# Kernel optimization log

Hardware: AMD Instinct MI355X
Metric: run time of the kernel (lower is better)

Reference implementation:

```python
import jax, jax.numpy as jnp
import numpy as np

D_MODEL = 1024
HIDDEN = 4096
NUM_EXPERTS = 8
NUM_GROUPS = 4      # from _compute_group_size(4, 4096) with max_group_size=4096
GROUP_SIZE = 4096
EXPERT_CAPACITY = 512  # round(1.0 * 4096 / 8), >= max(8, 4096//100)


def setup_inputs() -> dict:
    key = jax.random.key(0)
    ks = jax.random.split(key, 10)
    s_in = 1.0 / np.sqrt(D_MODEL)
    s_hid = 1.0 / np.sqrt(HIDDEN)
    return {
        "x": jax.random.normal(ks[0], (4, 4096, D_MODEL), dtype=jnp.float32),
        "gate_w": jax.random.normal(ks[1], (D_MODEL, NUM_EXPERTS), dtype=jnp.float32) * 0.1,
        "gate_b": jax.random.normal(ks[2], (NUM_EXPERTS,), dtype=jnp.float32) * 0.01,
        "temperature": jnp.ones((1,), dtype=jnp.float32),
        "shared_w1": jax.random.normal(ks[3], (D_MODEL, HIDDEN), dtype=jnp.float32) * s_in,
        "shared_b1": jnp.zeros((HIDDEN,), dtype=jnp.float32),
        "shared_w2": jax.random.normal(ks[4], (HIDDEN, D_MODEL), dtype=jnp.float32) * s_hid,
        "shared_b2": jnp.zeros((D_MODEL,), dtype=jnp.float32),
        "expert_w1": jax.random.normal(ks[5], (NUM_EXPERTS, D_MODEL, HIDDEN), dtype=jnp.float32) * s_in,
        "expert_b1": jnp.zeros((NUM_EXPERTS, HIDDEN), dtype=jnp.float32),
        "expert_w2": jax.random.normal(ks[6], (NUM_EXPERTS, HIDDEN, D_MODEL), dtype=jnp.float32) * s_hid,
        "expert_b2": jnp.zeros((NUM_EXPERTS, D_MODEL), dtype=jnp.float32),
    }


def reference(x, gate_w, gate_b, temperature, shared_w1, shared_b1, shared_w2,
              shared_b2, expert_w1, expert_b1, expert_w2, expert_b2):
    B, S, D = x.shape
    T = NUM_GROUPS * GROUP_SIZE  # total tokens (no padding here)
    xg = x.reshape(NUM_GROUPS, GROUP_SIZE, D)

    # Router: softmax over temperature-scaled gate logits
    logits = jnp.einsum('gsd,de->gse', xg, gate_w) + gate_b
    safe_temp = jnp.maximum(temperature, 0.1)
    probs = jax.nn.softmax(logits / safe_temp, axis=-1)  # [G, Gs, E]
    # per-expert top-k over ALL tokens (flattened across groups)
    flat_probs = probs.transpose(2, 0, 1).reshape(NUM_EXPERTS, T)
    scores, tok_idx = jax.lax.top_k(flat_probs, EXPERT_CAPACITY)  # [E, C]

    # Shared expert FFN (gelu is tanh-approx, matching flax nn.gelu default)
    shared = jnp.einsum('gsh,hd->gsd',
                        jax.nn.gelu(jnp.einsum('gsd,dh->gsh', xg, shared_w1) + shared_b1),
                        shared_w2) + shared_b2

    # Routed experts: gather tokens, grouped FFN, weighted scatter-add
    x_flat = xg.reshape(T, D)
    tokens = x_flat[tok_idx]  # [E, C, D]
    h = jax.nn.gelu(jnp.einsum('ecd,edh->ech', tokens, expert_w1) + expert_b1[:, None, :])
    out_e = jnp.einsum('ech,ehd->ecd', h, expert_w2) + expert_b2[:, None, :]
    out_e = out_e * scores[..., None]
    routed = jnp.zeros_like(x_flat).at[tok_idx.reshape(-1)].add(out_e.reshape(-1, D))

    out = shared.reshape(T, D) + routed
    return out.reshape(B, S, D)
```

## Files before the change

kernel.cpp:

```cpp
#include <hip/hip_runtime.h>

#define NTOK 16384
#define DMODEL 1024
#define DHID 4096
#define NEXP 8
#define CAP 512

typedef __attribute__((ext_vector_type(8))) short bfrag_t;
typedef __attribute__((ext_vector_type(4))) float ffrag_t;
typedef __attribute__((ext_vector_type(4))) unsigned int u32x4;

__device__ __forceinline__ unsigned short f2bf(float f) {
  unsigned u = __float_as_uint(f);
  u += 0x7FFFu + ((u >> 16) & 1u);
  return (unsigned short)(u >> 16);
}

__device__ __forceinline__ float gelu_fast(float x) {
  float t = x * x;
  float z = x * fmaf(0.071354814f, t, 1.5957691f);
  float e = __expf(-z);
  return x * __builtin_amdgcn_rcpf(1.0f + e);
}

__global__ __launch_bounds__(256) void k_trans_all(const float* __restrict__ sw1,
                                                   const float* __restrict__ ew1,
                                                   const float* __restrict__ sw2,
                                                   const float* __restrict__ ew2,
                                                   unsigned short* __restrict__ w1t,
                                                   unsigned short* __restrict__ ew1t,
                                                   unsigned short* __restrict__ w2t,
                                                   unsigned short* __restrict__ ew2t) {
  const int zb = blockIdx.z;
  const float* in;
  unsigned short* out;
  int K, N, bx, by;
  if (zb < 9) {
    K = DMODEL; N = DHID;
    bx = blockIdx.x; by = blockIdx.y;
    if (zb == 0) { in = sw1; out = w1t; }
    else { in = ew1 + (size_t)(zb - 1) * K * N; out = ew1t + (size_t)(zb - 1) * N * K; }
  } else {
    K = DHID; N = DMODEL;
    const int id = blockIdx.y * 64 + blockIdx.x;
    bx = id & 15; by = id >> 4;
    if (zb == 9) { in = sw2; out = w2t; }
    else { in = ew2 + (size_t)(zb - 10) * K * N; out = ew2t + (size_t)(zb - 10) * N * K; }
  }
  __shared__ float tile[64][65];
  const int n0 = bx * 64, k0 = by * 64;
  const int tx = threadIdx.x & 63, ty = threadIdx.x >> 6;
#pragma unroll
  for (int i = 0; i < 16; ++i) {
    const int k = ty * 16 + i;
    tile[k][tx] = in[(size_t)(k0 + k) * N + n0 + tx];
  }
  __syncthreads();
  const int sx = threadIdx.x & 7, sy = threadIdx.x >> 3;
#pragma unroll
  for (int j = 0; j < 2; ++j) {
    const int n = sy + j * 32;
    u32x4 v;
    v.x = (unsigned)f2bf(tile[sx * 8 + 0][n]) | ((unsigned)f2bf(tile[sx * 8 + 1][n]) << 16);
    v.y = (unsigned)f2bf(tile[sx * 8 + 2][n]) | ((unsigned)f2bf(tile[sx * 8 + 3][n]) << 16);
    v.z = (unsigned)f2bf(tile[sx * 8 + 4][n]) | ((unsigned)f2bf(tile[sx * 8 + 5][n]) << 16);
    v.w = (unsigned)f2bf(tile[sx * 8 + 6][n]) | ((unsigned)f2bf(tile[sx * 8 + 7][n]) << 16);
    *(u32x4*)&out[(size_t)(n0 + n) * K + k0 + sx * 8] = v;
  }
}

__global__ __launch_bounds__(256) void k_router(const float* __restrict__ x, const float* __restrict__ gw,
                                                const float* __restrict__ gb, const float* __restrict__ temp,
                                                float* __restrict__ probs, unsigned short* __restrict__ xb) {
  __shared__ float gws[DMODEL * NEXP];
  for (int i = threadIdx.x; i < DMODEL * NEXP; i += 256) gws[i] = gw[i];
  __syncthreads();
  const int wave = threadIdx.x >> 6, lane = threadIdx.x & 63;
  const int t = blockIdx.x * 4 + wave;
  const float* xr = x + (size_t)t * DMODEL;
  unsigned short* xw = xb + (size_t)t * DMODEL;
  float acc[NEXP];
#pragma unroll
  for (int e = 0; e < NEXP; ++e) acc[e] = 0.f;
  for (int d = lane; d < DMODEL; d += 64) {
    float xv = xr[d];
    xw[d] = f2bf(xv);
#pragma unroll
    for (int e = 0; e < NEXP; ++e) acc[e] += xv * gws[d * NEXP + e];
  }
#pragma unroll
  for (int off = 32; off >= 1; off >>= 1) {
#pragma unroll
    for (int e = 0; e < NEXP; ++e) acc[e] += __shfl_xor(acc[e], off);
  }
  if (lane == 0) {
    float st = fmaxf(temp[0], 0.1f);
    float m = -1e30f;
#pragma unroll
    for (int e = 0; e < NEXP; ++e) { acc[e] = (acc[e] + gb[e]) / st; m = fmaxf(m, acc[e]); }
    float s = 0.f;
#pragma unroll
    for (int e = 0; e < NEXP; ++e) { acc[e] = expf(acc[e] - m); s += acc[e]; }
    float inv = 1.f / s;
#pragma unroll
    for (int e = 0; e < NEXP; ++e) probs[(size_t)e * NTOK + t] = acc[e] * inv;
  }
}

__global__ __launch_bounds__(1024) void k_topk(const float* __restrict__ probs, int* __restrict__ tok,
                                               float* __restrict__ scores, int* __restrict__ eqbuf,
                                               int* __restrict__ slot) {
  const int e = blockIdx.x;
  const float* p = probs + (size_t)e * NTOK;
  int* eq = eqbuf + (size_t)e * NTOK;
  int* sl = slot + (size_t)e * NTOK;
  __shared__ int hist[256];
  __shared__ unsigned sh_pref;
  __shared__ int sh_k, sh_gt, sh_eq, sh_cnt;
  const int tid = threadIdx.x;
  const int NTHR = 1024;
  for (int t = tid; t < NTOK; t += NTHR) sl[t] = -1;
  if (tid == 0) { sh_pref = 0u; sh_k = CAP; }
  __syncthreads();
  for (int pass = 3; pass >= 0; --pass) {
    if (tid < 256) hist[tid] = 0;
    __syncthreads();
    const unsigned pref = sh_pref;
    const int shift = pass * 8;
    for (int t = tid; t < NTOK; t += NTHR) {
      unsigned key = __float_as_uint(p[t]);
      bool cand = (pass == 3) || ((key >> (shift + 8)) == pref);
      if (cand) atomicAdd(&hist[(key >> shift) & 255], 1);
    }
    __syncthreads();
    if (tid == 0) {
      int k = sh_k;
      int d = 255;
      while (hist[d] < k) { k -= hist[d]; --d; }
      sh_k = k;
      sh_pref = (pref << 8) | (unsigned)d;
    }
    __syncthreads();
  }
  const unsigned Kstar = sh_pref;
  const int need_eq = sh_k;
  if (tid == 0) { sh_gt = 0; sh_eq = 0; }
  __syncthreads();
  for (int t = tid; t < NTOK; t += NTHR) {
    unsigned key = __float_as_uint(p[t]);
    if (key > Kstar) {
      int pos = atomicAdd(&sh_gt, 1);
      tok[e * CAP + pos] = t;
      scores[e * CAP + pos] = p[t];
      sl[t] = pos;
    } else if (key == Kstar) {
      int q = atomicAdd(&sh_eq, 1);
      eq[q] = t;
    }
  }
  __syncthreads();
  const int cg = sh_gt, ce = sh_eq;
  if (ce <= need_eq) {
    for (int j = tid; j < ce; j += NTHR) {
      tok[e * CAP + cg + j] = eq[j];
      scores[e * CAP + cg + j] = p[eq[j]];
      sl[eq[j]] = cg + j;
    }
  } else {
    int lo = 0, hi = NTOK - 1;
    while (lo < hi) {
      int mid = (lo + hi) >> 1;
      if (tid == 0) sh_cnt = 0;
      __syncthreads();
      for (int j = tid; j < ce; j += NTHR)
        if (eq[j] <= mid) atomicAdd(&sh_cnt, 1);
      __syncthreads();
      if (sh_cnt >= need_eq) hi = mid; else lo = mid + 1;
      __syncthreads();
    }
    if (tid == 0) sh_cnt = 0;
    __syncthreads();
    for (int j = tid; j < ce; j += NTHR) {
      if (eq[j] <= lo) {
        int pos = cg + atomicAdd(&sh_cnt, 1);
        tok[e * CAP + pos] = eq[j];
        scores[e * CAP + pos] = p[eq[j]];
        sl[eq[j]] = pos;
      }
    }
  }
}

template <int MODE, bool GATHER, bool NT>
__global__ __launch_bounds__(256, 4) void k_gemm(
    const unsigned short* __restrict__ A, const unsigned short* __restrict__ Bt,
    const float* __restrict__ bias, float* __restrict__ outF, unsigned short* __restrict__ outB,
    const int* __restrict__ tok, const float* __restrict__ scale,
    int M, int N, int Kloop, int LDK, int ksplit) {
  const int zb = blockIdx.z / ksplit;
  const int kc = blockIdx.z % ksplit;
  if (!GATHER) A += (size_t)zb * M * LDK;
  A += (size_t)kc * Kloop;
  Bt += (size_t)zb * N * LDK + (size_t)kc * Kloop;
  const float* bz = bias + (size_t)zb * N;

  const int gx = gridDim.x, gy = gridDim.y;
  const int nwg = gx * gy;
  const int id = blockIdx.x + blockIdx.y * gx;
  int bx, by;
  if ((gx & 7) == 0) {
    const int x = id & 7, c = id >> 3, H = gx >> 3;
    bx = x * H + (c % H);
    by = c / H;
  } else if ((nwg & 7) == 0) {
    const int q = nwg >> 3;
    const int sw = (id & 7) * q + (id >> 3);
    bx = sw % gx;
    by = sw / gx;
  } else {
    bx = blockIdx.x;
    by = blockIdx.y;
  }
  const int m0 = bx * 128, n0 = by * 128;

  const int tid = threadIdx.x, wave = tid >> 6, lane = tid & 63;
  const int wm = (wave >> 1) * 64, wn = (wave & 1) * 64;

  __shared__ alignas(16) unsigned short sh[128 * 128];
  unsigned short* As = sh;
  unsigned short* Bs = sh + 128 * 64;

  ffrag_t acc[4][4];
#pragma unroll
  for (int i = 0; i < 4; ++i)
#pragma unroll
    for (int j = 0; j < 4; ++j)
#pragma unroll
      for (int r = 0; r < 4; ++r) acc[i][j][r] = 0.f;

  int lb[4];
  const unsigned short* rowA[4];
  const unsigned short* rowB[4];
#pragma unroll
  for (int it = 0; it < 4; ++it) {
    int L = it * 256 + tid;
    int rr = L >> 3;
    int gg = (L & 7) ^ (rr & 7);
    lb[it] = (it * 256 + wave * 64) * 16;
    const unsigned short* ab =
        GATHER ? (A + (size_t)tok[zb * M + m0 + rr] * LDK) : (A + (size_t)(m0 + rr) * LDK);
    rowA[it] = ab + gg * 8;
    rowB[it] = Bt + (size_t)(n0 + rr) * LDK + gg * 8;
  }

  for (int kt = 0; kt < Kloop; kt += 64) {
#pragma unroll
    for (int it = 0; it < 4; ++it) {
      __builtin_amdgcn_global_load_lds(
          (const __attribute__((address_space(1))) unsigned int*)(rowA[it] + kt),
          (__attribute__((address_space(3))) unsigned int*)((char*)As + lb[it]), 16, 0, 0);
      __builtin_amdgcn_global_load_lds(
          (const __attribute__((address_space(1))) unsigned int*)(rowB[it] + kt),
          (__attribute__((address_space(3))) unsigned int*)((char*)Bs + lb[it]), 16, 0, 0);
    }
    __syncthreads();
#pragma unroll
    for (int kk = 0; kk < 2; ++kk) {
      bfrag_t af[4], bf[4];
      const int gl = kk * 4 + (lane >> 4);
#pragma unroll
      for (int mi = 0; mi < 4; ++mi) {
        int r = wm + mi * 16 + (lane & 15);
        af[mi] = *(const bfrag_t*)&As[r * 64 + ((gl ^ (r & 7)) * 8)];
      }
#pragma unroll
      for (int ni = 0; ni < 4; ++ni) {
        int r = wn + ni * 16 + (lane & 15);
        bf[ni] = *(const bfrag_t*)&Bs[r * 64 + ((gl ^ (r & 7)) * 8)];
      }
#pragma unroll
      for (int mi = 0; mi < 4; ++mi)
#pragma unroll
        for (int ni = 0; ni < 4; ++ni)
          acc[mi][ni] = __builtin_amdgcn_mfma_f32_16x16x32_bf16(af[mi], bf[ni], acc[mi][ni], 0, 0, 0);
    }
    __syncthreads();
  }

  const int rsub = (lane >> 4) * 4, cs = lane & 15;
  if (MODE == 0) {
    float bv[4];
#pragma unroll
    for (int ni = 0; ni < 4; ++ni) bv[ni] = bz[n0 + wn + ni * 16 + cs];
#pragma unroll
    for (int mi = 0; mi < 4; ++mi)
#pragma unroll
      for (int ni = 0; ni < 4; ++ni)
#pragma unroll
        for (int r = 0; r < 4; ++r) {
          float v = acc[mi][ni][r] + bv[ni];
          sh[(wm + mi * 16 + rsub + r) * 128 + (wn + ni * 16 + cs)] = f2bf(gelu_fast(v));
        }
    __syncthreads();
    const int seg = tid & 15, rw = tid >> 4;
#pragma unroll
    for (int rep = 0; rep < 8; ++rep) {
      const int row = rep * 16 + rw;
      u32x4 v = *(const u32x4*)&sh[row * 128 + seg * 8];
      u32x4* dst = (u32x4*)&outB[((size_t)zb * M + m0 + row) * N + n0 + seg * 8];
      if (NT)
        __builtin_nontemporal_store(v, dst);
      else
        *dst = v;
    }
  } else if (MODE == 3) {
    float* po = outF + (size_t)blockIdx.z * M * N;
#pragma unroll
    for (int ni = 0; ni < 4; ++ni) {
      const int n = n0 + wn + ni * 16 + cs;
      const float bv = (kc == 0) ? bz[n] : 0.f;
#pragma unroll
      for (int mi = 0; mi < 4; ++mi)
#pragma unroll
        for (int r = 0; r < 4; ++r) {
          const int m = m0 + wm + mi * 16 + rsub + r;
          const float s = scale[zb * M + m];
          po[(size_t)m * N + n] = (acc[mi][ni][r] + bv) * s;
        }
    }
  } else {
    const int* slot = tok;
    const float* pe = scale;
    float bv[4];
#pragma unroll
    for (int ni = 0; ni < 4; ++ni) bv[ni] = bz[n0 + wn + ni * 16 + cs];
#pragma unroll
    for (int mi = 0; mi < 4; ++mi) {
#pragma unroll
      for (int r = 0; r < 4; ++r) {
        const int m = m0 + wm + mi * 16 + rsub + r;
        float ex[4] = {0.f, 0.f, 0.f, 0.f};
#pragma unroll
        for (int e = 0; e < NEXP; ++e) {
          const int sl = slot[(size_t)e * NTOK + m];
          if (sl >= 0) {
            const float* p0 = pe + ((size_t)(e * 2 + 0) * CAP + sl) * DMODEL;
            const float* p1 = pe + ((size_t)(e * 2 + 1) * CAP + sl) * DMODEL;
#pragma unroll
            for (int ni = 0; ni < 4; ++ni) {
              const int n = n0 + wn + ni * 16 + cs;
              ex[ni] += p0[n] + p1[n];
            }
          }
        }
#pragma unroll
        for (int ni = 0; ni < 4; ++ni) {
          const int n = n0 + wn + ni * 16 + cs;
          __builtin_nontemporal_store(acc[mi][ni][r] + bv[ni] + ex[ni],
                                      &outF[(size_t)m * N + n]);
        }
      }
    }
  }
}

extern "C" void kernel_launch(void* const* d_in, const int* in_sizes, int n_in,
                              void* d_out, int out_size, void* d_ws, size_t ws_size,
                              hipStream_t stream) {
  const float* x      = (const float*)d_in[0];
  const float* gate_w = (const float*)d_in[1];
  const float* gate_b = (const float*)d_in[2];
  const float* temp   = (const float*)d_in[3];
  const float* sw1    = (const float*)d_in[4];
  const float* sb1    = (const float*)d_in[5];
  const float* sw2    = (const float*)d_in[6];
  const float* sb2    = (const float*)d_in[7];
  const float* ew1    = (const float*)d_in[8];
  const float* eb1    = (const float*)d_in[9];
  const float* ew2    = (const float*)d_in[10];
  const float* eb2    = (const float*)d_in[11];
  float* out = (float*)d_out;

  char* ws = (char*)d_ws;
  size_t o = 0;
  auto take = [&](size_t bytes) { char* p = ws + o; o += (bytes + 255) & ~(size_t)255; return p; };
  unsigned short* x_bf = (unsigned short*)take((size_t)NTOK * DMODEL * 2);
  unsigned short* w1t  = (unsigned short*)take((size_t)DMODEL * DHID * 2);
  unsigned short* w2t  = (unsigned short*)take((size_t)DHID * DMODEL * 2);
  unsigned short* ew1t = (unsigned short*)take((size_t)NEXP * DMODEL * DHID * 2);
  unsigned short* ew2t = (unsigned short*)take((size_t)NEXP * DHID * DMODEL * 2);
  float* probs         = (float*)take((size_t)NEXP * NTOK * 4);
  int* tok             = (int*)take((size_t)NEXP * CAP * 4);
  float* scores        = (float*)take((size_t)NEXP * CAP * 4);
  int* eqbuf           = (int*)take((size_t)NEXP * NTOK * 4);
  int* slot            = (int*)take((size_t)NEXP * NTOK * 4);
  float* pe            = (float*)take((size_t)NEXP * 2 * CAP * DMODEL * 4);
  unsigned short* he   = (unsigned short*)take((size_t)NEXP * CAP * DHID * 2);
  unsigned short* hs   = (unsigned short*)take((size_t)NTOK * DHID * 2);

  k_trans_all<<<dim3(64, 16, 18), 256, 0, stream>>>(sw1, ew1, sw2, ew2, w1t, ew1t, w2t, ew2t);

  k_router<<<NTOK / 4, 256, 0, stream>>>(x, gate_w, gate_b, temp, probs, x_bf);
  k_topk<<<NEXP, 1024, 0, stream>>>(probs, tok, scores, eqbuf, slot);

  k_gemm<0, false, false><<<dim3(128, 32, 1), 256, 0, stream>>>(
      x_bf, w1t, sb1, nullptr, hs, nullptr, nullptr, NTOK, DHID, DMODEL, DMODEL, 1);

  k_gemm<0, true, false><<<dim3(4, 32, NEXP), 256, 0, stream>>>(
      x_bf, ew1t, eb1, nullptr, he, tok, nullptr, CAP, DHID, DMODEL, DMODEL, 1);
  k_gemm<3, false, false><<<dim3(4, 8, NEXP * 2), 256, 0, stream>>>(
      he, ew2t, eb2, pe, nullptr, nullptr, scores, CAP, DMODEL, DHID / 2, DHID, 2);

  k_gemm<4, false, true><<<dim3(128, 8, 1), 256, 0, stream>>>(
      hs, w2t, sb2, out, nullptr, slot, pe, NTOK, DMODEL, DHID, DHID, 1);
}
```

Measured before the change: 612.1 us.

## Merge weight transpose with router and shared/expert first GEMMs into single launches

```diff
diff --git a/kernel.cpp b/kernel.cpp
--- a/kernel.cpp
+++ b/kernel.cpp
@@ -23,87 +23,87 @@
   return x * __builtin_amdgcn_rcpf(1.0f + e);
 }
 
-__global__ __launch_bounds__(256) void k_trans_all(const float* __restrict__ sw1,
-                                                   const float* __restrict__ ew1,
-                                                   const float* __restrict__ sw2,
-                                                   const float* __restrict__ ew2,
-                                                   unsigned short* __restrict__ w1t,
-                                                   unsigned short* __restrict__ ew1t,
-                                                   unsigned short* __restrict__ w2t,
-                                                   unsigned short* __restrict__ ew2t) {
-  const int zb = blockIdx.z;
-  const float* in;
-  unsigned short* out;
-  int K, N, bx, by;
-  if (zb < 9) {
-    K = DMODEL; N = DHID;
-    bx = blockIdx.x; by = blockIdx.y;
-    if (zb == 0) { in = sw1; out = w1t; }
-    else { in = ew1 + (size_t)(zb - 1) * K * N; out = ew1t + (size_t)(zb - 1) * N * K; }
+__global__ __launch_bounds__(256) void k_prep(
+    const float* __restrict__ sw1, const float* __restrict__ ew1,
+    const float* __restrict__ sw2, const float* __restrict__ ew2,
+    unsigned short* __restrict__ w1t, unsigned short* __restrict__ ew1t,
+    unsigned short* __restrict__ w2t, unsigned short* __restrict__ ew2t,
+    const float* __restrict__ x, const float* __restrict__ gw,
+    const float* __restrict__ gb, const float* __restrict__ temp,
+    float* __restrict__ probs, unsigned short* __restrict__ xb) {
+  __shared__ char smem[32768];
+  const int id = blockIdx.x;
+  if (id < 18432) {
+    float(*tile)[65] = (float(*)[65])smem;
+    const int zb = id >> 10, r = id & 1023;
+    const float* in;
+    unsigned short* out;
+    int K, N, bx, by;
+    if (zb < 9) {
+      K = DMODEL; N = DHID;
+      bx = r & 63; by = r >> 6;
+      if (zb == 0) { in = sw1; out = w1t; }
+      else { in = ew1 + (size_t)(zb - 1) * K * N; out = ew1t + (size_t)(zb - 1) * N * K; }
+    } else {
+      K = DHID; N = DMODEL;
+      bx = r & 15; by = r >> 4;
+      if (zb == 9) { in = sw2; out = w2t; }
+      else { in = ew2 + (size_t)(zb - 10) * K * N; out = ew2t + (size_t)(zb - 10) * N * K; }
+    }
+    const int n0 = bx * 64, k0 = by * 64;
+    const int tx = threadIdx.x & 63, ty = threadIdx.x >> 6;
+#pragma unroll
+    for (int i = 0; i < 16; ++i) {
+      const int k = ty * 16 + i;
+      tile[k][tx] = in[(size_t)(k0 + k) * N + n0 + tx];
+    }
+    __syncthreads();
+    const int sx = threadIdx.x & 7, sy = threadIdx.x >> 3;
+#pragma unroll
+    for (int j = 0; j < 2; ++j) {
+      const int n = sy + j * 32;
+      u32x4 v;
+      v.x = (unsigned)f2bf(tile[sx * 8 + 0][n]) | ((unsigned)f2bf(tile[sx * 8 + 1][n]) << 16);
+      v.y = (unsigned)f2bf(tile[sx * 8 + 2][n]) | ((unsigned)f2bf(tile[sx * 8 + 3][n]) << 16);
+      v.z = (unsigned)f2bf(tile[sx * 8 + 4][n]) | ((unsigned)f2bf(tile[sx * 8 + 5][n]) << 16);
+      v.w = (unsigned)f2bf(tile[sx * 8 + 6][n]) | ((unsigned)f2bf(tile[sx * 8 + 7][n]) << 16);
+      *(u32x4*)&out[(size_t)(n0 + n) * K + k0 + sx * 8] = v;
+    }
   } else {
-    K = DHID; N = DMODEL;
-    const int id = blockIdx.y * 64 + blockIdx.x;
-    bx = id & 15; by = id >> 4;
-    if (zb == 9) { in = sw2; out = w2t; }
-    else { in = ew2 + (size_t)(zb - 10) * K * N; out = ew2t + (size_t)(zb - 10) * N * K; }
-  }
-  __shared__ float tile[64][65];
-  const int n0 = bx * 64, k0 = by * 64;
-  const int tx = threadIdx.x & 63, ty = threadIdx.x >> 6;
-#pragma unroll
-  for (int i = 0; i < 16; ++i) {
-    const int k = ty * 16 + i;
-    tile[k][tx] = in[(size_t)(k0 + k) * N + n0 + tx];
-  }
-  __syncthreads();
-  const int sx = threadIdx.x & 7, sy = threadIdx.x >> 3;
-#pragma unroll
-  for (int j = 0; j < 2; ++j) {
-    const int n = sy + j * 32;
-    u32x4 v;
-    v.x = (unsigned)f2bf(tile[sx * 8 + 0][n]) | ((unsigned)f2bf(tile[sx * 8 + 1][n]) << 16);
-    v.y = (unsigned)f2bf(tile[sx * 8 + 2][n]) | ((unsigned)f2bf(tile[sx * 8 + 3][n]) << 16);
-    v.z = (unsigned)f2bf(tile[sx * 8 + 4][n]) | ((unsigned)f2bf(tile[sx * 8 + 5][n]) << 16);
-    v.w = (unsigned)f2bf(tile[sx * 8 + 6][n]) | ((unsigned)f2bf(tile[sx * 8 + 7][n]) << 16);
-    *(u32x4*)&out[(size_t)(n0 + n) * K + k0 + sx * 8] = v;
-  }
-}
-
-__global__ __launch_bounds__(256) void k_router(const float* __restrict__ x, const float* __restrict__ gw,
-                                                const float* __restrict__ gb, const float* __restrict__ temp,
-                                                float* __restrict__ probs, unsigned short* __restrict__ xb) {
-  __shared__ float gws[DMODEL * NEXP];
-  for (int i = threadIdx.x; i < DMODEL * NEXP; i += 256) gws[i] = gw[i];
-  __syncthreads();
-  const int wave = threadIdx.x >> 6, lane = threadIdx.x & 63;
-  const int t = blockIdx.x * 4 + wave;
-  const float* xr = x + (size_t)t * DMODEL;
-  unsigned short* xw = xb + (size_t)t * DMODEL;
-  float acc[NEXP];
-#pragma unroll
-  for (int e = 0; e < NEXP; ++e) acc[e] = 0.f;
-  for (int d = lane; d < DMODEL; d += 64) {
-    float xv = xr[d];
-    xw[d] = f2bf(xv);
-#pragma unroll
-    for (int e = 0; e < NEXP; ++e) acc[e] += xv * gws[d * NEXP + e];
-  }
-#pragma unroll
-  for (int off = 32; off >= 1; off >>= 1) {
-#pragma unroll
-    for (int e = 0; e < NEXP; ++e) acc[e] += __shfl_xor(acc[e], off);
-  }
-  if (lane == 0) {
-    float st = fmaxf(temp[0], 0.1f);
-    float m = -1e30f;
-#pragma unroll
-    for (int e = 0; e < NEXP; ++e) { acc[e] = (acc[e] + gb[e]) / st; m = fmaxf(m, acc[e]); }
-    float s = 0.f;
-#pragma unroll
-    for (int e = 0; e < NEXP; ++e) { acc[e] = expf(acc[e] - m); s += acc[e]; }
-    float inv = 1.f / s;
-#pragma unroll
-    for (int e = 0; e < NEXP; ++e) probs[(size_t)e * NTOK + t] = acc[e] * inv;
+    float* gws = (float*)smem;
+    const int rb = id - 18432;
+    for (int i = threadIdx.x; i < DMODEL * NEXP; i += 256) gws[i] = gw[i];
+    __syncthreads();
+    const int wave = threadIdx.x >> 6, lane = threadIdx.x & 63;
+    const int t = rb * 4 + wave;
+    const float* xr = x + (size_t)t * DMODEL;
+    unsigned short* xw = xb + (size_t)t * DMODEL;
+    float acc[NEXP];
+#pragma unroll
+    for (int e = 0; e < NEXP; ++e) acc[e] = 0.f;
+    for (int d = lane; d < DMODEL; d += 64) {
+      float xv = xr[d];
+      xw[d] = f2bf(xv);
+#pragma unroll
+      for (int e = 0; e < NEXP; ++e) acc[e] += xv * gws[d * NEXP + e];
+    }
+#pragma unroll
+    for (int off = 32; off >= 1; off >>= 1) {
+#pragma unroll
+      for (int e = 0; e < NEXP; ++e) acc[e] += __shfl_xor(acc[e], off);
+    }
+    if (lane == 0) {
+      float st = fmaxf(temp[0], 0.1f);
+      float m = -1e30f;
+#pragma unroll
+      for (int e = 0; e < NEXP; ++e) { acc[e] = (acc[e] + gb[e]) / st; m = fmaxf(m, acc[e]); }
+      float s = 0.f;
+#pragma unroll
+      for (int e = 0; e < NEXP; ++e) { acc[e] = expf(acc[e] - m); s += acc[e]; }
+      float inv = 1.f / s;
+#pragma unroll
+      for (int e = 0; e < NEXP; ++e) probs[(size_t)e * NTOK + t] = acc[e] * inv;
+    }
   }
 }
 
@@ -191,6 +191,119 @@
   }
 }
 
+__global__ __launch_bounds__(256, 4) void k_gemm1(
+    const unsigned short* __restrict__ xb,
+    const unsigned short* __restrict__ w1t, const unsigned short* __restrict__ ew1t,
+    const float* __restrict__ sb1, const float* __restrict__ eb1,
+    unsigned short* __restrict__ hs, unsigned short* __restrict__ he,
+    const int* __restrict__ tok) {
+  const int id = blockIdx.x;
+  int m0, n0, gmode, tbase = 0;
+  const unsigned short* Bt;
+  const float* bz;
+  unsigned short* outB;
+  if (id < 4096) {
+    const int x = id & 7, c = id >> 3;
+    m0 = (x * 16 + (c & 15)) * 128;
+    n0 = (c >> 4) * 128;
+    Bt = w1t; bz = sb1; outB = hs; gmode = 0;
+  } else {
+    const int rid = id - 4096;
+    const int e = rid >> 7, r = rid & 127;
+    m0 = (r & 3) * 128;
+    n0 = (r >> 2) * 128;
+    Bt = ew1t + (size_t)e * (DHID * DMODEL);
+    bz = eb1 + (size_t)e * DHID;
+    outB = he + (size_t)e * (CAP * DHID);
+    gmode = 1;
+    tbase = e * CAP;
+  }
+  const int tid = threadIdx.x, wave = tid >> 6, lane = tid & 63;
+  const int wm = (wave >> 1) * 64, wn = (wave & 1) * 64;
+
+  __shared__ alignas(16) unsigned short sh[128 * 128];
+  unsigned short* As = sh;
+  unsigned short* Bs = sh + 128 * 64;
+
+  ffrag_t acc[4][4];
+#pragma unroll
+  for (int i = 0; i < 4; ++i)
+#pragma unroll
+    for (int j = 0; j < 4; ++j)
+#pragma unroll
+      for (int r = 0; r < 4; ++r) acc[i][j][r] = 0.f;
+
+  int lb[4];
+  const unsigned short* rowA[4];
+  const unsigned short* rowB[4];
+#pragma unroll
+  for (int it = 0; it < 4; ++it) {
+    int L = it * 256 + tid;
+    int rr = L >> 3;
+    int gg = (L & 7) ^ (rr & 7);
+    lb[it] = (it * 256 + wave * 64) * 16;
+    const int arow = gmode ? tok[tbase + m0 + rr] : (m0 + rr);
+    rowA[it] = xb + (size_t)arow * DMODEL + gg * 8;
+    rowB[it] = Bt + (size_t)(n0 + rr) * DMODEL + gg * 8;
+  }
+
+  for (int kt = 0; kt < DMODEL; kt += 64) {
+#pragma unroll
+    for (int it = 0; it < 4; ++it) {
+      __builtin_amdgcn_global_load_lds(
+          (const __attribute__((address_space(1))) unsigned int*)(rowA[it] + kt),
+          (__attribute__((address_space(3))) unsigned int*)((char*)As + lb[it]), 16, 0, 0);
+      __builtin_amdgcn_global_load_lds(
+          (const __attribute__((address_space(1))) unsigned int*)(rowB[it] + kt),
+          (__attribute__((address_space(3))) unsigned int*)((char*)Bs + lb[it]), 16, 0, 0);
+    }
+    __syncthreads();
+#pragma unroll
+    for (int kk = 0; kk < 2; ++kk) {
+      bfrag_t af[4], bf[4];
+      const int gl = kk * 4 + (lane >> 4);
+#pragma unroll
+      for (int mi = 0; mi < 4; ++mi) {
+        int r = wm + mi * 16 + (lane & 15);
+        af[mi] = *(const bfrag_t*)&As[r * 64 + ((gl ^ (r & 7)) * 8)];
+      }
+#pragma unroll
+      for (int ni = 0; ni < 4; ++ni) {
+        int r = wn + ni * 16 + (lane & 15);
+        bf[ni] = *(const bfrag_t*)&Bs[r * 64 + ((gl ^ (r & 7)) * 8)];
+      }
+#pragma unroll
+      for (int mi = 0; mi < 4; ++mi)
+#pragma unroll
+        for (int ni = 0; ni < 4; ++ni)
+          acc[mi][ni] = __builtin_amdgcn_mfma_f32_16x16x32_bf16(af[mi], bf[ni], acc[mi][ni], 0, 0, 0);
+    }
+    __syncthreads();
+  }
+
+  const int rsub = (lane >> 4) * 4, cs = lane & 15;
+  float bv[4];
+#pragma unroll
+  for (int ni = 0; ni < 4; ++ni) bv[ni] = bz[n0 + wn + ni * 16 + cs];
+#pragma unroll
+  for (int mi = 0; mi < 4; ++mi)
+#pragma unroll
+    for (int ni = 0; ni < 4; ++ni)
+#pragma unroll
+      for (int r = 0; r < 4; ++r) {
+        float v = acc[mi][ni][r] + bv[ni];
+        sh[(wm + mi * 16 + rsub + r) * 128 + (wn + ni * 16 + cs)] = f2bf(gelu_fast(v));
+      }
+  __syncthreads();
+  const int seg = tid & 15, rw = tid >> 4;
+#pragma unroll
+  for (int rep = 0; rep < 8; ++rep) {
+    const int row = rep * 16 + rw;
+    u32x4 v = *(const u32x4*)&sh[row * 128 + seg * 8];
+    *(u32x4*)&outB[(size_t)(m0 + row) * DHID + n0 + seg * 8] = v;
+  }
+}
+
 template <int MODE, bool GATHER, bool NT>
 __global__ __launch_bounds__(256, 4) void k_gemm(
     const unsigned short* __restrict__ A, const unsigned short* __restrict__ Bt,
@@ -288,32 +401,7 @@
   }
 
   const int rsub = (lane >> 4) * 4, cs = lane & 15;
-  if (MODE == 0) {
-    float bv[4];
-#pragma unroll
-    for (int ni = 0; ni < 4; ++ni) bv[ni] = bz[n0 + wn + ni * 16 + cs];
-#pragma unroll
-    for (int mi = 0; mi < 4; ++mi)
-#pragma unroll
-      for (int ni = 0; ni < 4; ++ni)
-#pragma unroll
-        for (int r = 0; r < 4; ++r) {
-          float v = acc[mi][ni][r] + bv[ni];
-          sh[(wm + mi * 16 + rsub + r) * 128 + (wn + ni * 16 + cs)] = f2bf(gelu_fast(v));
-        }
-    __syncthreads();
-    const int seg = tid & 15, rw = tid >> 4;
-#pragma unroll
-    for (int rep = 0; rep < 8; ++rep) {
-      const int row = rep * 16 + rw;
-      u32x4 v = *(const u32x4*)&sh[row * 128 + seg * 8];
-      u32x4* dst = (u32x4*)&outB[((size_t)zb * M + m0 + row) * N + n0 + seg * 8];
-      if (NT)
-        __builtin_nontemporal_store(v, dst);
-      else
-        *dst = v;
-    }
-  } else if (MODE == 3) {
+  if (MODE == 3) {
     float* po = outF + (size_t)blockIdx.z * M * N;
 #pragma unroll
     for (int ni = 0; ni < 4; ++ni) {
@@ -398,16 +486,13 @@
   unsigned short* he   = (unsigned short*)take((size_t)NEXP * CAP * DHID * 2);
   unsigned short* hs   = (unsigned short*)take((size_t)NTOK * DHID * 2);
 
-  k_trans_all<<<dim3(64, 16, 18), 256, 0, stream>>>(sw1, ew1, sw2, ew2, w1t, ew1t, w2t, ew2t);
-
-  k_router<<<NTOK / 4, 256, 0, stream>>>(x, gate_w, gate_b, temp, probs, x_bf);
+  k_prep<<<18432 + 4096, 256, 0, stream>>>(sw1, ew1, sw2, ew2, w1t, ew1t, w2t, ew2t,
+                                           x, gate_w, gate_b, temp, probs, x_bf);
+
   k_topk<<<NEXP, 1024, 0, stream>>>(probs, tok, scores, eqbuf, slot);
 
-  k_gemm<0, false, false><<<dim3(128, 32, 1), 256, 0, stream>>>(
-      x_bf, w1t, sb1, nullptr, hs, nullptr, nullptr, NTOK, DHID, DMODEL, DMODEL, 1);
-
-  k_gemm<0, true, false><<<dim3(4, 32, NEXP), 256, 0, stream>>>(
-      x_bf, ew1t, eb1, nullptr, he, tok, nullptr, CAP, DHID, DMODEL, DMODEL, 1);
+  k_gemm1<<<4096 + NEXP * 128, 256, 0, stream>>>(x_bf, w1t, ew1t, sb1, eb1, hs, he, tok);
+
   k_gemm<3, false, false><<<dim3(4, 8, NEXP * 2), 256, 0, stream>>>(
       he, ew2t, eb2, pe, nullptr, nullptr, scores, CAP, DMODEL, DHID / 2, DHID, 2);
 
```

Result: slower. 717.2 us (+17.2%).
